# Kernel optimization log

Hardware: AMD Instinct MI355X
Metric: run time of the kernel (lower is better)

## Reference

```python
import jax, jax.numpy as jnp
import numpy as np

B, T, D, H, E = 4, 2048, 1024, 4096, 8


def setup_inputs() -> dict:
    key = jax.random.key(0)
    ks = jax.random.split(key, 7)
    x = jax.random.normal(ks[0], (B, T, D), dtype=jnp.float32)
    # Gate: Linear(D, E)
    Wg = jax.random.normal(ks[1], (D, E), dtype=jnp.float32) / np.sqrt(D)
    bg = jax.random.normal(ks[2], (E,), dtype=jnp.float32) * 0.01
    # Experts: E x [Linear(D,H), ReLU, Linear(H,D)] (dropout inactive at eval)
    W1 = jax.random.normal(ks[3], (E, D, H), dtype=jnp.float32) / np.sqrt(D)
    b1 = jax.random.normal(ks[4], (E, H), dtype=jnp.float32) * 0.01
    W2 = jax.random.normal(ks[5], (E, H, D), dtype=jnp.float32) / np.sqrt(H)
    b2 = jax.random.normal(ks[6], (E, D), dtype=jnp.float32) * 0.01
    return {"x": x, "Wg": Wg, "bg": bg, "W1": W1, "b1": b1, "W2": W2, "b2": b2}


def reference(x, Wg, bg, W1, b1, W2, b2):
    # Gate + hard top-1 routing
    gate_scores = x @ Wg + bg                      # [B,T,E]
    top1 = jnp.argmax(gate_scores, axis=-1)        # [B,T]
    onehot = jax.nn.one_hot(top1, Wg.shape[-1], dtype=x.dtype)  # [B,T,E]
    # Dense: every expert MLP over all tokens (matches original's masked
    # formulation: x*mask == x on selected tokens, output re-masked).
    h = jax.nn.relu(jnp.einsum('btd,edh->beth', x, W1) + b1[None, :, None, :])
    y = jnp.einsum('beth,ehd->betd', h, W2) + b2[None, :, None, :]
    # Masked combine: keep only the token's chosen expert output
    out = jnp.einsum('betd,bte->btd', y, onehot)
    return out
```

## Files before the change

### kernel.cpp

```cpp
#include <hip/hip_runtime.h>
#include <hip/hip_bf16.h>
#include <stdint.h>

#define NTOK 8192
#define DDIM 1024
#define HDIM 4096
#define NEXP 8
#define MAXWL1 48
#define MAXWL2 72

typedef __attribute__((ext_vector_type(4))) float f32x4;
typedef __attribute__((ext_vector_type(8))) short s16x8;
typedef __attribute__((ext_vector_type(8))) unsigned short u16x8;

__device__ __forceinline__ unsigned short f2bf(float f) {
  union { float f; unsigned int u; } v; v.f = f;
  unsigned int u = v.u;
  u += 0x7FFFu + ((u >> 16) & 1u);
  return (unsigned short)(u >> 16);
}

typedef __attribute__((address_space(3))) unsigned char lds_u8;
typedef const __attribute__((address_space(1))) unsigned char glb_u8;

__device__ __forceinline__ void load_lds16(const void* g, void* l) {
  __builtin_amdgcn_global_load_lds((glb_u8*)g, (lds_u8*)l, 16, 0, 0);
}

template <int VM> __device__ __forceinline__ void wait_vm() {
  if constexpr (VM == 6)      asm volatile("s_waitcnt vmcnt(6)" ::: "memory");
  else if constexpr (VM == 4) asm volatile("s_waitcnt vmcnt(4)" ::: "memory");
  else if constexpr (VM == 3) asm volatile("s_waitcnt vmcnt(3)" ::: "memory");
  else if constexpr (VM == 2) asm volatile("s_waitcnt vmcnt(2)" ::: "memory");
  else                        asm volatile("s_waitcnt vmcnt(0)" ::: "memory");
}

__global__ __launch_bounds__(256) void gate_kernel(
    const float* __restrict__ x, const float* __restrict__ Wg,
    const float* __restrict__ bg, int* __restrict__ counts,
    int* __restrict__ lists) {
  const int lane = threadIdx.x & 63;
  const int tok = blockIdx.x * 4 + (threadIdx.x >> 6);
  const float* xr = x + (size_t)tok * DDIM;
  double acc[NEXP];
#pragma unroll
  for (int e = 0; e < NEXP; ++e) acc[e] = 0.0;
#pragma unroll 4
  for (int it = 0; it < DDIM / 64; ++it) {
    const int d = it * 64 + lane;
    const float xv = xr[d];
    const f32x4 w0 = *(const f32x4*)(Wg + (size_t)d * NEXP);
    const f32x4 w1 = *(const f32x4*)(Wg + (size_t)d * NEXP + 4);
#pragma unroll
    for (int j = 0; j < 4; ++j) {
      acc[j]     += (double)xv * (double)w0[j];
      acc[4 + j] += (double)xv * (double)w1[j];
    }
  }
#pragma unroll
  for (int e = 0; e < NEXP; ++e) {
    double v = acc[e];
#pragma unroll
    for (int off = 32; off > 0; off >>= 1) v += __shfl_xor(v, off, 64);
    acc[e] = v;
  }
  if (lane == 0) {
    int best = 0;
    double bv = acc[0] + (double)bg[0];
#pragma unroll
    for (int e = 1; e < NEXP; ++e) {
      const double v = acc[e] + (double)bg[e];
      if (v > bv) { bv = v; best = e; }
    }
    const int pos = atomicAdd(&counts[best], 1);
    lists[best * NTOK + pos] = tok;
  }
}

__global__ void offs_kernel(const int* __restrict__ counts, int* __restrict__ offs,
                            int* __restrict__ wl1, int* __restrict__ wl2) {
  int s = 0;
#pragma unroll
  for (int e = 0; e < NEXP; ++e) { offs[e] = s; s += counts[e]; }
  offs[NEXP] = s;
  int n1 = 0, n2 = 0;
  for (int e = 0; e < NEXP; ++e) {
    const int nb1 = (counts[e] + 255) >> 8;
    for (int b = 0; b < nb1; ++b) wl1[n1++] = (e << 20) | b;
    const int nb2 = (counts[e] + 127) >> 7;
    for (int b = 0; b < nb2; ++b) wl2[n2++] = (e << 20) | b;
  }
  offs[NEXP + 1] = n1;
  offs[NEXP + 2] = n2;
}

__global__ __launch_bounds__(256) void gather_conv_kernel(
    const float* __restrict__ x, const int* __restrict__ offs,
    const int* __restrict__ lists, int* __restrict__ stok,
    unsigned short* __restrict__ xbs) {
  const int p = blockIdx.x * 4 + (threadIdx.x >> 6);
  const int lane = threadIdx.x & 63;
  int e = 0;
#pragma unroll
  for (int k = 1; k < NEXP; ++k) e += (p >= offs[k]) ? 1 : 0;
  const int tok = lists[e * NTOK + (p - offs[e])];
  if (lane == 0) stok[p] = tok;
  const float* src = x + (size_t)tok * DDIM + lane * 16;
  unsigned short* dst = xbs + (size_t)p * DDIM + lane * 16;
#pragma unroll
  for (int q = 0; q < 2; ++q) {
    const f32x4 a = *(const f32x4*)(src + q * 8);
    const f32x4 b = *(const f32x4*)(src + q * 8 + 4);
    u16x8 o;
#pragma unroll
    for (int j = 0; j < 4; ++j) { o[j] = f2bf(a[j]); o[4 + j] = f2bf(b[j]); }
    *(u16x8*)(dst + q * 8) = o;
  }
}

__global__ __launch_bounds__(256) void transpose_conv_kernel(
    const float* __restrict__ in, unsigned short* __restrict__ out,
    int R, int C) {
  __shared__ __align__(16) unsigned short T[64][68];
  const int e = blockIdx.z;
  const float* ine = in + (size_t)e * R * C;
  unsigned short* oute = out + (size_t)e * C * R;
  const int c0 = blockIdx.x * 64, r0 = blockIdx.y * 64;
  const int t = threadIdx.x;
  const int rb = (t >> 4) * 4;
  const int cb = (t & 15) * 4;
  f32x4 v[4];
#pragma unroll
  for (int j = 0; j < 4; ++j)
    v[j] = *(const f32x4*)(ine + (size_t)(r0 + rb + j) * C + c0 + cb);
#pragma unroll
  for (int i = 0; i < 4; ++i) {
    ushort4 o;
    o.x = f2bf(v[0][i]); o.y = f2bf(v[1][i]);
    o.z = f2bf(v[2][i]); o.w = f2bf(v[3][i]);
    *(ushort4*)&T[cb + i][rb] = o;
  }
  __syncthreads();
  const int c = t >> 2, q = (t & 3) * 16;
  u16x8 o0, o1;
#pragma unroll
  for (int j = 0; j < 8; ++j) { o0[j] = T[c][q + j]; o1[j] = T[c][q + 8 + j]; }
  *(u16x8*)(oute + (size_t)(c0 + c) * R + r0 + q) = o0;
  *(u16x8*)(oute + (size_t)(c0 + c) * R + r0 + q + 8) = o1;
}

template <int BM, int BN, int WM, int WN, int K, int N, int MAXWLT,
          bool COLFAST, bool FUSE1>
__global__ __launch_bounds__(512, 4) void ffn_kernel(
    const unsigned short* __restrict__ A, const unsigned short* __restrict__ Bt,
    const float* __restrict__ bias, const int* __restrict__ counts,
    const int* __restrict__ offs, const int* __restrict__ wl,
    const int* __restrict__ stok, unsigned short* __restrict__ outb,
    float* __restrict__ outf, int nwl_idx) {
  constexpr int MF = BM / (WM * 16);
  constexpr int NF = BN / (WN * 16);
  constexpr int ISS_A = BM / 128;
  constexpr int ISS_B = BN / 128;
  constexpr int S = ISS_A + ISS_B;
  constexpr int NT = K / 32;
  constexpr int NCB = N / BN;
  constexpr int NWG = NCB * MAXWLT;
  static_assert((NWG & 7) == 0 && (NT % 3) == 2 && NT >= 5, "");
  static_assert(WM * WN == 8, "8 waves");

  const int d = blockIdx.x;
  const int logical = (d & 7) * (NWG / 8) + (d >> 3);
  int cb, wli;
  if constexpr (COLFAST) { cb = logical % NCB; wli = logical / NCB; }
  else                   { cb = logical / MAXWLT; wli = logical % MAXWLT; }
  if (wli >= offs[nwl_idx]) return;
  const int col0 = cb * BN;
  const int wle = wl[wli];
  const int e = wle >> 20;
  const int bx = wle & 0xFFFFF;
  const int cnt = counts[e];
  const int row0 = offs[e] + bx * BM;

  __shared__ __align__(16) unsigned short As0[BM * 32], Bs0[BN * 32];
  __shared__ __align__(16) unsigned short As1[BM * 32], Bs1[BN * 32];
  __shared__ __align__(16) unsigned short As2[BM * 32], Bs2[BN * 32];

  const int tid = threadIdx.x;
  const int lane = tid & 63;
  const int w = tid >> 6;
  const int wm = w / WN;
  const int wn = w % WN;
  const int fr = lane & 15;
  const int fj = lane >> 4;

  const int swsrc = ((tid & 3) ^ ((tid >> 3) & 3)) * 8;
  const int rb = tid >> 2;
  const unsigned short* srcA[ISS_A];
#pragma unroll
  for (int i = 0; i < ISS_A; ++i) {
    int gr = row0 + i * 128 + rb;
    if (gr > NTOK - 1) gr = NTOK - 1;
    srcA[i] = A + (size_t)gr * K + swsrc;
  }
  const unsigned short* Bte = Bt + (size_t)e * N * K;
  const unsigned short* srcB[ISS_B];
#pragma unroll
  for (int i = 0; i < ISS_B; ++i)
    srcB[i] = Bte + (size_t)(col0 + i * 128 + rb) * K + swsrc;

  const int js = (fj ^ ((fr >> 1) & 3)) * 8;

  f32x4 acc[MF][NF];
#pragma unroll
  for (int m = 0; m < MF; ++m)
#pragma unroll
    for (int n = 0; n < NF; ++n) acc[m][n] = f32x4{0.f, 0.f, 0.f, 0.f};

  auto stage = [&](unsigned short* dA, unsigned short* dB, int kel) {
#pragma unroll
    for (int i = 0; i < ISS_A; ++i)
      load_lds16(srcA[i] + kel, dA + i * 4096 + tid * 8);
#pragma unroll
    for (int i = 0; i < ISS_B; ++i)
      load_lds16(srcB[i] + kel, dB + i * 4096 + tid * 8);
  };

  auto body = [&](const unsigned short* pA, const unsigned short* pB,
                  unsigned short* nA, unsigned short* nB, int knext,
                  bool do_stage) {
    __builtin_amdgcn_s_barrier();
    asm volatile("" ::: "memory");
    s16x8 af[MF], bf[NF];
#pragma unroll
    for (int m = 0; m < MF; ++m)
      af[m] = *(const s16x8*)(pA + (wm * MF * 16 + m * 16 + fr) * 32 + js);
#pragma unroll
    for (int n = 0; n < NF; ++n)
      bf[n] = *(const s16x8*)(pB + (wn * NF * 16 + n * 16 + fr) * 32 + js);
    if (do_stage) stage(nA, nB, knext);
    __builtin_amdgcn_s_setprio(1);
#pragma unroll
    for (int m = 0; m < MF; ++m)
#pragma unroll
      for (int n = 0; n < NF; ++n)
        acc[m][n] = __builtin_amdgcn_mfma_f32_16x16x32_bf16(af[m], bf[n],
                                                            acc[m][n], 0, 0, 0);
    __builtin_amdgcn_s_setprio(0);
  };

  stage(As0, Bs0, 0);
  stage(As1, Bs1, 32);

#pragma unroll 1
  for (int t = 0; t < NT - 2; t += 3) {
    wait_vm<S>(); body(As0, Bs0, As2, Bs2, (t + 2) * 32, true);
    wait_vm<S>(); body(As1, Bs1, As0, Bs0, (t + 3) * 32, true);
    wait_vm<S>(); body(As2, Bs2, As1, Bs1, (t + 4) * 32, true);
  }
  wait_vm<S>(); body(As0, Bs0, nullptr, nullptr, 0, false);
  wait_vm<0>(); body(As1, Bs1, nullptr, nullptr, 0, false);

#pragma unroll
  for (int n = 0; n < NF; ++n) {
    const int col = col0 + wn * NF * 16 + n * 16 + fr;
    const float bv = bias[e * N + col];
#pragma unroll
    for (int m = 0; m < MF; ++m) {
#pragma unroll
      for (int j = 0; j < 4; ++j) {
        const int rl = wm * MF * 16 + m * 16 + fj * 4 + j;
        if (bx * BM + rl < cnt) {
          if constexpr (FUSE1) {
            outb[(size_t)(row0 + rl) * N + col] = f2bf(fmaxf(acc[m][n][j] + bv, 0.f));
          } else {
            outf[(size_t)stok[row0 + rl] * N + col] = acc[m][n][j] + bv;
          }
        }
      }
    }
  }
}

extern "C" void kernel_launch(void* const* d_in, const int* in_sizes, int n_in,
                              void* d_out, int out_size, void* d_ws, size_t ws_size,
                              hipStream_t stream) {
  (void)in_sizes; (void)n_in; (void)out_size;
  const float* x  = (const float*)d_in[0];
  const float* Wg = (const float*)d_in[1];
  const float* bg = (const float*)d_in[2];
  const float* W1 = (const float*)d_in[3];
  const float* b1 = (const float*)d_in[4];
  const float* W2 = (const float*)d_in[5];
  const float* b2 = (const float*)d_in[6];
  float* out = (float*)d_out;

  char* ws = (char*)d_ws;
  const size_t OFF_CNT = 0;
  const size_t OFF_OFF = 128;
  const size_t OFF_WL1 = 256;
  const size_t OFF_WL2 = 256 + MAXWL1 * 4;
  const size_t OFF_LST = 1024;
  const size_t OFF_STK = OFF_LST + (size_t)NEXP * NTOK * 4;
  const size_t OFF_XBS = OFF_STK + (size_t)NTOK * 4;
  const size_t OFF_HS  = OFF_XBS + (size_t)NTOK * DDIM * 2;
  const size_t OFF_WT  = OFF_HS + (size_t)NTOK * HDIM * 2;
  const size_t NEED    = OFF_WT + (size_t)NEXP * DDIM * HDIM * 2;
  if (ws_size < NEED) return;

  int* counts = (int*)(ws + OFF_CNT);
  int* offs   = (int*)(ws + OFF_OFF);
  int* wl1    = (int*)(ws + OFF_WL1);
  int* wl2    = (int*)(ws + OFF_WL2);
  int* lists  = (int*)(ws + OFF_LST);
  int* stok   = (int*)(ws + OFF_STK);
  unsigned short* xbs = (unsigned short*)(ws + OFF_XBS);
  unsigned short* Hs  = (unsigned short*)(ws + OFF_HS);
  unsigned short* Wt  = (unsigned short*)(ws + OFF_WT);

  hipMemsetAsync(counts, 0, 128, stream);
  gate_kernel<<<NTOK / 4, 256, 0, stream>>>(x, Wg, bg, counts, lists);
  offs_kernel<<<1, 1, 0, stream>>>(counts, offs, wl1, wl2);
  gather_conv_kernel<<<NTOK / 4, 256, 0, stream>>>(x, offs, lists, stok, xbs);

  transpose_conv_kernel<<<dim3(HDIM / 64, DDIM / 64, NEXP), 256, 0, stream>>>(
      W1, Wt, DDIM, HDIM);
  ffn_kernel<256, 128, 4, 2, DDIM, HDIM, MAXWL1, false, true>
      <<<dim3((HDIM / 128) * MAXWL1), 512, 0, stream>>>(
          xbs, Wt, b1, counts, offs, wl1, stok, Hs, nullptr, NEXP + 1);
  transpose_conv_kernel<<<dim3(DDIM / 64, HDIM / 64, NEXP), 256, 0, stream>>>(
      W2, Wt, HDIM, DDIM);
  ffn_kernel<128, 256, 2, 4, HDIM, DDIM, MAXWL2, true, false>
      <<<dim3((DDIM / 256) * MAXWL2), 512, 0, stream>>>(
          Hs, Wt, b2, counts, offs, wl2, stok, nullptr, out, NEXP + 2);
}
```

Measured before the change: 457.6 us.

## Widen first FFN GEMM tile to 256x256 and use four-buffer LDS pipeline

Fixes the block N tile at 256 with a 2x4 wave grid. This raises the first expert GEMM tile from 256x128 to 256x256, halving its grid and increasing operand reuse per workgroup. The LDS staging changes from a three-buffer ring to four half-K buffers over 64-wide K steps, and launch bounds drop to 2 blocks per CU. The first GEMM now needs about 128KB of LDS, which limits occupancy to one block per CU and may hurt latency hiding.

```diff
diff --git a/kernel.cpp b/kernel.cpp
--- a/kernel.cpp
+++ b/kernel.cpp
@@ -28,10 +28,8 @@
 }
 
 template <int VM> __device__ __forceinline__ void wait_vm() {
-  if constexpr (VM == 6)      asm volatile("s_waitcnt vmcnt(6)" ::: "memory");
-  else if constexpr (VM == 4) asm volatile("s_waitcnt vmcnt(4)" ::: "memory");
+  if constexpr (VM == 4)      asm volatile("s_waitcnt vmcnt(4)" ::: "memory");
   else if constexpr (VM == 3) asm volatile("s_waitcnt vmcnt(3)" ::: "memory");
-  else if constexpr (VM == 2) asm volatile("s_waitcnt vmcnt(2)" ::: "memory");
   else                        asm volatile("s_waitcnt vmcnt(0)" ::: "memory");
 }
 
@@ -149,24 +147,23 @@
   *(u16x8*)(oute + (size_t)(c0 + c) * R + r0 + q + 8) = o1;
 }
 
-template <int BM, int BN, int WM, int WN, int K, int N, int MAXWLT,
-          bool COLFAST, bool FUSE1>
-__global__ __launch_bounds__(512, 4) void ffn_kernel(
+template <int BM, int K, int N, int MAXWLT, bool COLFAST, bool FUSE1>
+__global__ __launch_bounds__(512, 2) void ffn_kernel(
     const unsigned short* __restrict__ A, const unsigned short* __restrict__ Bt,
     const float* __restrict__ bias, const int* __restrict__ counts,
     const int* __restrict__ offs, const int* __restrict__ wl,
     const int* __restrict__ stok, unsigned short* __restrict__ outb,
     float* __restrict__ outf, int nwl_idx) {
-  constexpr int MF = BM / (WM * 16);
-  constexpr int NF = BN / (WN * 16);
+  constexpr int BN = 256;
+  constexpr int MF = BM / 32;
+  constexpr int NF = 4;
   constexpr int ISS_A = BM / 128;
-  constexpr int ISS_B = BN / 128;
+  constexpr int ISS_B = 2;
   constexpr int S = ISS_A + ISS_B;
-  constexpr int NT = K / 32;
+  constexpr int NT = K / 64;
   constexpr int NCB = N / BN;
   constexpr int NWG = NCB * MAXWLT;
-  static_assert((NWG & 7) == 0 && (NT % 3) == 2 && NT >= 5, "");
-  static_assert(WM * WN == 8, "8 waves");
+  static_assert((NWG & 7) == 0 && (NT & 1) == 0 && NT >= 4, "");
 
   const int d = blockIdx.x;
   const int logical = (d & 7) * (NWG / 8) + (d >> 3);
@@ -181,15 +178,16 @@
   const int cnt = counts[e];
   const int row0 = offs[e] + bx * BM;
 
-  __shared__ __align__(16) unsigned short As0[BM * 32], Bs0[BN * 32];
-  __shared__ __align__(16) unsigned short As1[BM * 32], Bs1[BN * 32];
-  __shared__ __align__(16) unsigned short As2[BM * 32], Bs2[BN * 32];
+  __shared__ __align__(16) unsigned short A00[BM * 32], A01[BM * 32];
+  __shared__ __align__(16) unsigned short A10[BM * 32], A11[BM * 32];
+  __shared__ __align__(16) unsigned short B00[BN * 32], B01[BN * 32];
+  __shared__ __align__(16) unsigned short B10[BN * 32], B11[BN * 32];
 
   const int tid = threadIdx.x;
   const int lane = tid & 63;
   const int w = tid >> 6;
-  const int wm = w / WN;
-  const int wn = w % WN;
+  const int wr = w >> 2;
+  const int wc = w & 3;
   const int fr = lane & 15;
   const int fj = lane >> 4;
 
@@ -225,19 +223,19 @@
       load_lds16(srcB[i] + kel, dB + i * 4096 + tid * 8);
   };
 
-  auto body = [&](const unsigned short* pA, const unsigned short* pB,
-                  unsigned short* nA, unsigned short* nB, int knext,
-                  bool do_stage) {
+  auto phase = [&](const unsigned short* pA, const unsigned short* pB,
+                   unsigned short* nA, unsigned short* nB, int kel,
+                   bool do_stage) {
     __builtin_amdgcn_s_barrier();
     asm volatile("" ::: "memory");
     s16x8 af[MF], bf[NF];
 #pragma unroll
     for (int m = 0; m < MF; ++m)
-      af[m] = *(const s16x8*)(pA + (wm * MF * 16 + m * 16 + fr) * 32 + js);
+      af[m] = *(const s16x8*)(pA + (wr * MF * 16 + m * 16 + fr) * 32 + js);
 #pragma unroll
     for (int n = 0; n < NF; ++n)
-      bf[n] = *(const s16x8*)(pB + (wn * NF * 16 + n * 16 + fr) * 32 + js);
-    if (do_stage) stage(nA, nB, knext);
+      bf[n] = *(const s16x8*)(pB + (wc * 64 + n * 16 + fr) * 32 + js);
+    if (do_stage) stage(nA, nB, kel);
     __builtin_amdgcn_s_setprio(1);
 #pragma unroll
     for (int m = 0; m < MF; ++m)
@@ -248,27 +246,30 @@
     __builtin_amdgcn_s_setprio(0);
   };
 
-  stage(As0, Bs0, 0);
-  stage(As1, Bs1, 32);
+  stage(A00, B00, 0);
+  stage(A01, B01, 32);
 
 #pragma unroll 1
-  for (int t = 0; t < NT - 2; t += 3) {
-    wait_vm<S>(); body(As0, Bs0, As2, Bs2, (t + 2) * 32, true);
-    wait_vm<S>(); body(As1, Bs1, As0, Bs0, (t + 3) * 32, true);
-    wait_vm<S>(); body(As2, Bs2, As1, Bs1, (t + 4) * 32, true);
-  }
-  wait_vm<S>(); body(As0, Bs0, nullptr, nullptr, 0, false);
-  wait_vm<0>(); body(As1, Bs1, nullptr, nullptr, 0, false);
+  for (int t = 0; t < NT - 2; t += 2) {
+    wait_vm<S>(); phase(A00, B00, A10, B10, (t + 1) * 64,      true);
+    wait_vm<S>(); phase(A01, B01, A11, B11, (t + 1) * 64 + 32, true);
+    wait_vm<S>(); phase(A10, B10, A00, B00, (t + 2) * 64,      true);
+    wait_vm<S>(); phase(A11, B11, A01, B01, (t + 2) * 64 + 32, true);
+  }
+  wait_vm<S>(); phase(A00, B00, A10, B10, (NT - 1) * 64,      true);
+  wait_vm<S>(); phase(A01, B01, A11, B11, (NT - 1) * 64 + 32, true);
+  wait_vm<S>(); phase(A10, B10, nullptr, nullptr, 0, false);
+  wait_vm<0>(); phase(A11, B11, nullptr, nullptr, 0, false);
 
 #pragma unroll
   for (int n = 0; n < NF; ++n) {
-    const int col = col0 + wn * NF * 16 + n * 16 + fr;
+    const int col = col0 + wc * 64 + n * 16 + fr;
     const float bv = bias[e * N + col];
 #pragma unroll
     for (int m = 0; m < MF; ++m) {
 #pragma unroll
       for (int j = 0; j < 4; ++j) {
-        const int rl = wm * MF * 16 + m * 16 + fj * 4 + j;
+        const int rl = wr * MF * 16 + m * 16 + fj * 4 + j;
         if (bx * BM + rl < cnt) {
           if constexpr (FUSE1) {
             outb[(size_t)(row0 + rl) * N + col] = f2bf(fmaxf(acc[m][n][j] + bv, 0.f));
@@ -324,12 +325,12 @@
 
   transpose_conv_kernel<<<dim3(HDIM / 64, DDIM / 64, NEXP), 256, 0, stream>>>(
       W1, Wt, DDIM, HDIM);
-  ffn_kernel<256, 128, 4, 2, DDIM, HDIM, MAXWL1, false, true>
-      <<<dim3((HDIM / 128) * MAXWL1), 512, 0, stream>>>(
+  ffn_kernel<256, DDIM, HDIM, MAXWL1, false, true>
+      <<<dim3((HDIM / 256) * MAXWL1), 512, 0, stream>>>(
           xbs, Wt, b1, counts, offs, wl1, stok, Hs, nullptr, NEXP + 1);
   transpose_conv_kernel<<<dim3(DDIM / 64, HDIM / 64, NEXP), 256, 0, stream>>>(
       W2, Wt, HDIM, DDIM);
-  ffn_kernel<128, 256, 2, 4, HDIM, DDIM, MAXWL2, true, false>
+  ffn_kernel<128, HDIM, DDIM, MAXWL2, true, false>
       <<<dim3((DDIM / 256) * MAXWL2), 512, 0, stream>>>(
           Hs, Wt, b2, counts, offs, wl2, stok, nullptr, out, NEXP + 2);
 }
```

Result: slower. 531.9 us (+16.2%).
